# Performance work log

Hardware: AMD Instinct MI355X
Metric: run time of the kernel (lower is better)

Reference implementation:

```python
import jax, jax.numpy as jnp
import numpy as np
from functools import partial

G, NG, H, M, MC = 8, 256, 128, 128, 64
N, S = G * NG, H
TWO_PI = 2.0 * np.pi


def setup_inputs() -> dict:
    key = jax.random.key(0)
    ks = jax.random.split(key, 10)
    node_feat = jax.random.normal(ks[0], (N, S), jnp.float32)
    positions = jax.random.uniform(ks[1], (N, 3), jnp.float32) * 10.0
    # near-orthorhombic triclinic cells, safely invertible
    cell = 10.0 * jnp.eye(3, dtype=jnp.float32)[None] + 0.5 * jax.random.normal(ks[2], (G, 3, 3), jnp.float32)
    batch = jnp.repeat(jnp.arange(G, dtype=jnp.int32), NG)
    n_vecs = jax.random.randint(ks[3], (G, M, 3), -8, 9, dtype=jnp.int32)  # integer lattice vectors
    w = jax.random.uniform(ks[4], (G, M), jnp.float32)  # Ewald k-space weights (positive)
    W_qkv = jax.random.normal(ks[5], (3 * H, H), jnp.float32) / np.sqrt(H)
    W_vg = jax.random.normal(ks[6], (H, H), jnp.float32) / np.sqrt(H)
    b_vg = jnp.full((H,), 2.0, jnp.float32)
    W_hg = jax.random.normal(ks[7], (1, H), jnp.float32) / np.sqrt(H)
    b_hg = jnp.zeros((1,), jnp.float32)
    W_mg = jax.random.normal(ks[8], (1, H), jnp.float32) / np.sqrt(H)
    b_mg = jnp.full((1,), -5.0, jnp.float32)
    return dict(node_feat=node_feat, positions=positions, cell=cell, w=w,
                W_qkv=W_qkv, W_vg=W_vg, b_vg=b_vg, W_hg=W_hg, b_hg=b_hg,
                W_mg=W_mg, b_mg=b_mg, n_vecs=n_vecs, batch=batch)


def reference(node_feat, positions, cell, w, W_qkv, W_vg, b_vg, W_hg, b_hg, W_mg, b_mg, n_vecs, batch):
    Ntot, Sdim = node_feat.shape
    Gn = cell.shape[0]
    Ng = Ntot // Gn
    Hd = Sdim  # in_proj is Identity (S == hidden)
    dtype = node_feat.dtype
    scale_q = np.float32(1.0 / np.sqrt(Hd))

    scalars = node_feat
    qkv = scalars @ W_qkv.T                      # (N, 3H)
    q, k, v = jnp.split(qkv, 3, axis=-1)
    q = jax.nn.silu(q)
    k = jax.nn.silu(k)
    v = v * jax.nn.sigmoid(scalars @ W_vg.T + b_vg)

    # per-graph blocks (batch is block-contiguous: arange(G) repeated NG times)
    qg = q.reshape(Gn, Ng, Hd)
    kg = k.reshape(Gn, Ng, Hd)
    vg = v.reshape(Gn, Ng, Hd)
    a_q, b_q = qg[..., 0::2], qg[..., 1::2]      # (G, Ng, H/2)
    a_k, b_k = kg[..., 0::2], kg[..., 1::2]

    pos_g = positions.reshape(Gn, Ng, 3)
    # fractional coords: solve(cell^T, pos^T)^T, wrapped to [0,1)
    f = jax.vmap(lambda c, p: jnp.linalg.solve(c.T, p.T).T)(cell, pos_g)
    f = f - jnp.floor(f)                         # (G, Ng, 3)

    Mtot = n_vecs.shape[1]
    n_chunks = Mtot // MC
    n_f = n_vecs.astype(dtype)
    # (n_chunks, G, MC, ...) chunk streams for scan over k-space blocks
    n_xs = n_f.reshape(Gn, n_chunks, MC, 3).swapaxes(0, 1)
    w_xs = w.reshape(Gn, n_chunks, MC).swapaxes(0, 1)
    Ng_f = jnp.asarray(Ng, dtype)

    @jax.checkpoint
    def chunk(upd, xs):
        nb, wb = xs                              # (G, MC, 3), (G, MC)
        phase = TWO_PI * jnp.einsum('gni,gmi->gmn', f, nb)   # (G, MC, Ng)
        cos = jnp.cos(phase)[..., None]          # (G, MC, Ng, 1)
        sin = jnp.sin(phase)[..., None]
        aq, bq = a_q[:, None], b_q[:, None]      # (G, 1, Ng, H/2)
        ak, bk = a_k[:, None], b_k[:, None]
        q_rot = jnp.concatenate([aq * cos - bq * sin, aq * sin + bq * cos], -1) * scale_q  # (G,MC,Ng,H)
        k_rot = jnp.concatenate([ak * cos - bk * sin, ak * sin + bk * cos], -1)
        S_blk = jnp.einsum('gmnh,gnd->gmhd', k_rot, vg) / Ng_f   # (G, MC, H, H)
        beta = jnp.einsum('gmnh,gmhd->gmnd', q_rot, S_blk)       # (G, MC, Ng, H)
        upd = upd + jnp.einsum('gm,gmnd->gnd', wb, beta)
        return upd, None

    upd0 = jnp.zeros((Gn, Ng, Hd), dtype)
    upd, _ = jax.lax.scan(chunk, upd0, (n_xs, w_xs))
    update = upd.reshape(Ntot, Hd)

    attn_gate = jnp.tanh(scalars @ W_hg.T + b_hg)      # (N, 1)
    update = update * (1.0 + 0.2 * attn_gate)
    gate_sr_lr = jax.nn.sigmoid(scalars @ W_mg.T + b_mg)
    return update, gate_sr_lr
```

## Files before the change

kernel.cpp:

```cpp
#include <hip/hip_runtime.h>
#include <math.h>

using short8 = __attribute__((ext_vector_type(8))) short;
using f32x4 = __attribute__((ext_vector_type(4))) float;

#define MFMA16(a, b, c) __builtin_amdgcn_mfma_f32_16x16x32_bf16((a), (b), (c), 0, 0, 0)

namespace {
constexpr int NG_ = 256;
constexpr int H_ = 128;
constexpr int NTOT_ = 2048;
constexpr float SCALE_E = 0.08838834764831845f / 256.0f;

constexpr size_t OFF_QA = 0;
constexpr size_t OFF_KA = 524288;
constexpr size_t OFF_VT = 1048576;
constexpr size_t OFF_CT = 1572864;
constexpr size_t OFF_ST = 2097152;
constexpr size_t OFF_GF = 2621440;
}

__device__ __forceinline__ short f2bf(float x) {
  unsigned u = __float_as_uint(x);
  unsigned r = (u + 0x7FFFu + ((u >> 16) & 1u)) >> 16;
  return (short)r;
}
__device__ __forceinline__ float bf2f(short x) {
  return __uint_as_float(((unsigned)(unsigned short)x) << 16);
}
__device__ __forceinline__ float sigmoidf_(float x) { return 1.0f / (1.0f + expf(-x)); }
__device__ __forceinline__ float siluf_(float x) { return x / (1.0f + expf(-x)); }

__device__ __forceinline__ short8 neg8(short8 x) {
  short8 r;
#pragma unroll
  for (int i = 0; i < 8; ++i) r[i] = (short)(x[i] ^ (short)0x8000);
  return r;
}
__device__ __forceinline__ short8 ldf(const short* buf, int row, int kk) {
  return *(const short8*)&buf[(row * 128 + kk) ^ ((row & 7) << 3)];
}
__device__ __forceinline__ short8 ldf64(const short* buf, int row, int kk) {
  return *(const short8*)&buf[(row * 64 + kk) ^ ((row & 7) << 3)];
}

__global__ __launch_bounds__(512) void k_prep(
    const float* __restrict__ nf, const float* __restrict__ Wqkv,
    const float* __restrict__ Wvg, const float* __restrict__ bvg,
    const float* __restrict__ Whg, const float* __restrict__ bhg,
    const float* __restrict__ Wmg, const float* __restrict__ bmg,
    const float* __restrict__ cell, const float* __restrict__ pos,
    const int* __restrict__ nvec, const float* __restrict__ w,
    short* __restrict__ QA, short* __restrict__ KA, short* __restrict__ VT,
    short* __restrict__ CT, short* __restrict__ ST, float* __restrict__ GF,
    float* __restrict__ out_gate, float* __restrict__ out_zero) {
  __shared__ short smem[40960];
  const int tid = threadIdx.x;
  const int bid = blockIdx.x;
  if (bid < 64) {
    short* lA = smem;
    short* lB = smem + 8192;
    const int r_tile = bid >> 1, h = bid & 1;
    const int n0 = r_tile * 64, c0 = h * 256;
#pragma unroll
    for (int it = 0; it < 2; ++it) {
      int e = tid + it * 512;
      int row = e >> 4, c8 = (e & 15) * 8;
      const float* src = nf + (size_t)(n0 + row) * H_ + c8;
      float4 lo = *(const float4*)src, hi = *(const float4*)(src + 4);
      short8 v;
      v[0] = f2bf(lo.x); v[1] = f2bf(lo.y); v[2] = f2bf(lo.z); v[3] = f2bf(lo.w);
      v[4] = f2bf(hi.x); v[5] = f2bf(hi.y); v[6] = f2bf(hi.z); v[7] = f2bf(hi.w);
      *(short8*)&lA[(row * 128 + c8) ^ ((row & 7) << 3)] = v;
    }
#pragma unroll
    for (int it = 0; it < 8; ++it) {
      int e = tid + it * 512;
      int row = e >> 4, c8 = (e & 15) * 8;
      int wr_g = c0 + row;
      const float* src =
          (wr_g < 384 ? Wqkv + (size_t)wr_g * H_ : Wvg + (size_t)(wr_g - 384) * H_) + c8;
      float4 lo = *(const float4*)src, hi = *(const float4*)(src + 4);
      short8 v;
      v[0] = f2bf(lo.x); v[1] = f2bf(lo.y); v[2] = f2bf(lo.z); v[3] = f2bf(lo.w);
      v[4] = f2bf(hi.x); v[5] = f2bf(hi.y); v[6] = f2bf(hi.z); v[7] = f2bf(hi.w);
      *(short8*)&lB[(row * 128 + c8) ^ ((row & 7) << 3)] = v;
    }
    __syncthreads();
    const int wid = tid >> 6, lane = tid & 63;
    const int wrow = (wid >> 2) * 32, wcol = (wid & 3) * 64;
    const int frow = lane & 15, kq = (lane >> 4) * 8;
    f32x4 acc[2][4] = {};
#pragma unroll
    for (int ks = 0; ks < 4; ++ks) {
      int kk = ks * 32 + kq;
      short8 a[2], b[4];
#pragma unroll
      for (int i = 0; i < 2; ++i) a[i] = ldf(lA, wrow + i * 16 + frow, kk);
#pragma unroll
      for (int j = 0; j < 4; ++j) b[j] = ldf(lB, wcol + j * 16 + frow, kk);
#pragma unroll
      for (int i = 0; i < 2; ++i)
#pragma unroll
        for (int j = 0; j < 4; ++j) acc[i][j] = MFMA16(a[i], b[j], acc[i][j]);
    }
    const int orow = (lane >> 4) * 4, ocol = lane & 15;
    __syncthreads();
    if (h == 0) {
#pragma unroll
      for (int i = 0; i < 2; ++i)
#pragma unroll
        for (int j = 0; j < 4; ++j) {
          int c = wcol + j * 16 + ocol;
#pragma unroll
          for (int r = 0; r < 4; ++r) {
            int node = n0 + wrow + i * 16 + orow + r;
            float val = siluf_(acc[i][j][r]);
            if (c < 128)
              QA[(size_t)node * 128 + (c & 1) * 64 + (c >> 1)] = f2bf(val);
            else {
              int ck = c - 128;
              KA[(size_t)node * 128 + (ck & 1) * 64 + (ck >> 1)] = f2bf(val);
            }
          }
        }
    } else {
      short* gate_sh = lB;
      short* vt_sh = lB + 8192;
      if (wcol >= 128) {
#pragma unroll
        for (int i = 0; i < 2; ++i)
#pragma unroll
          for (int j = 0; j < 4; ++j) {
            int d = wcol - 128 + j * 16 + ocol;
#pragma unroll
            for (int r = 0; r < 4; ++r) {
              int nl = wrow + i * 16 + orow + r;
              gate_sh[nl * 128 + d] = f2bf(sigmoidf_(acc[i][j][r] + bvg[d]));
            }
          }
      }
      __syncthreads();
      if (wcol < 128) {
#pragma unroll
        for (int i = 0; i < 2; ++i)
#pragma unroll
          for (int j = 0; j < 4; ++j) {
            int d = wcol + j * 16 + ocol;
#pragma unroll
            for (int r = 0; r < 4; ++r) {
              int nl = wrow + i * 16 + orow + r;
              float gate = bf2f(gate_sh[nl * 128 + d]);
              vt_sh[(d * 64 + nl) ^ ((d & 7) << 3)] = f2bf(acc[i][j][r] * gate);
            }
          }
      }
      __syncthreads();
      const int g_idx = n0 >> 8, nbase = n0 & 255;
#pragma unroll
      for (int it = 0; it < 2; ++it) {
        int e = tid + it * 512;
        int d = e >> 3, n8 = (e & 7) * 8;
        short8 v = *(const short8*)&vt_sh[(d * 64 + n8) ^ ((d & 7) << 3)];
        *(short8*)&VT[((size_t)(g_idx * 128 + d)) * 256 + nbase + n8] = v;
      }
      if (tid < 64) {
        int nl = tid;
        float hg = 0.f, mg = 0.f;
#pragma unroll 8
        for (int c = 0; c < 128; ++c) {
          float s = bf2f(lA[((nl * 128 + (c & ~7)) ^ ((nl & 7) << 3)) + (c & 7)]);
          hg += s * Whg[c];
          mg += s * Wmg[c];
        }
        int node = n0 + nl;
        GF[node] = 1.0f + 0.2f * tanhf(hg + bhg[0]);
        out_gate[node] = sigmoidf_(mg + bmg[0]);
      }
    }
  } else {
    const int b = bid - 64;
    const int g = b >> 3, n0 = (b & 7) * 32;
    {
      float4 z = {0.f, 0.f, 0.f, 0.f};
      float* oz = out_zero + (size_t)b * 4096 + tid * 8;
      *(float4*)oz = z;
      *(float4*)(oz + 4) = z;
    }
    float* f_sh = (float*)smem;
    int* nv_sh = (int*)((char*)smem + 512);
    float* w_sh = (float*)((char*)smem + 2048);
    if (tid < 32) {
      const float* cg = cell + (size_t)g * 9;
      float A00 = cg[0], A01 = cg[3], A02 = cg[6];
      float A10 = cg[1], A11 = cg[4], A12 = cg[7];
      float A20 = cg[2], A21 = cg[5], A22 = cg[8];
      float b00 = A11 * A22 - A12 * A21;
      float b01 = A02 * A21 - A01 * A22;
      float b02 = A01 * A12 - A02 * A11;
      float b10 = A12 * A20 - A10 * A22;
      float b11 = A00 * A22 - A02 * A20;
      float b12 = A02 * A10 - A00 * A12;
      float b20 = A10 * A21 - A11 * A20;
      float b21 = A01 * A20 - A00 * A21;
      float b22 = A00 * A11 - A01 * A10;
      float det = A00 * b00 + A01 * b10 + A02 * b20;
      float inv = 1.0f / det;
      const int node = g * NG_ + n0 + tid;
      float p0 = pos[(size_t)node * 3 + 0];
      float p1 = pos[(size_t)node * 3 + 1];
      float p2 = pos[(size_t)node * 3 + 2];
      float f0 = (b00 * p0 + b01 * p1 + b02 * p2) * inv;
      float f1 = (b10 * p0 + b11 * p1 + b12 * p2) * inv;
      float f2 = (b20 * p0 + b21 * p1 + b22 * p2) * inv;
      f_sh[tid * 4 + 0] = f0 - floorf(f0);
      f_sh[tid * 4 + 1] = f1 - floorf(f1);
      f_sh[tid * 4 + 2] = f2 - floorf(f2);
    }
    if (tid < 128) {
      nv_sh[tid * 3 + 0] = nvec[((size_t)g * 128 + tid) * 3 + 0];
      nv_sh[tid * 3 + 1] = nvec[((size_t)g * 128 + tid) * 3 + 1];
      nv_sh[tid * 3 + 2] = nvec[((size_t)g * 128 + tid) * 3 + 2];
      w_sh[tid] = sqrtf(w[(size_t)g * 128 + tid]);
    }
    __syncthreads();
    const int n_l = tid >> 4, m0 = (tid & 15) * 8;
    float f0 = f_sh[n_l * 4 + 0], f1 = f_sh[n_l * 4 + 1], f2 = f_sh[n_l * 4 + 2];
    short8 pc, ps;
#pragma unroll
    for (int i = 0; i < 8; ++i) {
      int m = m0 + i;
      float dot = f0 * (float)nv_sh[m * 3] + f1 * (float)nv_sh[m * 3 + 1] +
                  f2 * (float)nv_sh[m * 3 + 2];
      float tr = dot - floorf(dot);
      float sn = __builtin_amdgcn_sinf(tr);
      float cs = __builtin_amdgcn_cosf(tr);
      float sq = w_sh[m];
      pc[i] = f2bf(sq * cs);
      ps[i] = f2bf(sq * sn);
    }
    const int node = g * NG_ + n0 + n_l;
    *(short8*)&CT[(size_t)node * 128 + m0] = pc;
    *(short8*)&ST[(size_t)node * 128 + m0] = ps;
  }
}

__global__ __launch_bounds__(512) void k_EV2(
    const short* __restrict__ QA, const short* __restrict__ KA,
    const short* __restrict__ VT, const short* __restrict__ CT,
    const short* __restrict__ ST, const float* __restrict__ GF,
    float* __restrict__ out) {
  __shared__ short smem[47104];
  short* tQ  = smem;
  short* tCr = smem + 4096;
  short* tSr = smem + 8192;
  short* tKA = smem + 12288;
  short* tCc = smem + 20480;
  short* tSc = smem + 28672;
  short* tV  = smem + 36864;
  short* tE  = smem + 45056;
  const int tid = threadIdx.x;
  const int bid = blockIdx.x;
  const int g = bid >> 5;
  const int rt = (bid >> 2) & 7;
  const int cc = bid & 3;
  const int R0 = rt * 32, C0 = cc * 64;
  const int gn = g * NG_;
  const int wid = tid >> 6, lane = tid & 63;
  const int frow = lane & 15, kq = (lane >> 4) * 8;
  const int orow = (lane >> 4) * 4, ocol = lane & 15;
  const int rfrag = wid >> 2;
  const int cfrag = wid & 3;

  {
    int row = tid >> 4, c8 = (tid & 15) * 8;
    int idx = (row * 128 + c8) ^ ((row & 7) << 3);
    size_t ga = (size_t)(gn + R0 + row) * 128 + c8;
    *(short8*)&tQ[idx] = *(const short8*)&QA[ga];
    *(short8*)&tCr[idx] = *(const short8*)&CT[ga];
    *(short8*)&tSr[idx] = *(const short8*)&ST[ga];
  }
#pragma unroll
  for (int it = 0; it < 2; ++it) {
    int e = tid + it * 512;
    int row = e >> 4, c8 = (e & 15) * 8;
    int idx = (row * 128 + c8) ^ ((row & 7) << 3);
    size_t ga = (size_t)(gn + C0 + row) * 128 + c8;
    *(short8*)&tKA[idx] = *(const short8*)&KA[ga];
    *(short8*)&tCc[idx] = *(const short8*)&CT[ga];
    *(short8*)&tSc[idx] = *(const short8*)&ST[ga];
    int d = e >> 3, n8 = (e & 7) * 8;
    *(short8*)&tV[(d * 64 + n8) ^ ((d & 7) << 3)] =
        *(const short8*)&VT[((size_t)g * 128 + d) * 256 + C0 + n8];
  }
  __syncthreads();
  f32x4 gc = {}, gs = {}, qc = {}, qs = {};
#pragma unroll
  for (int ks = 0; ks < 4; ++ks) {
    int kk = ks * 32 + kq, kk2 = (kk + 64) & 127;
    short8 aq = ldf(tQ, rfrag * 16 + frow, kk);
    short8 ka = ldf(tKA, cfrag * 16 + frow, kk);
    short8 t = ldf(tKA, cfrag * 16 + frow, kk2);
    short8 kb = (ks >= 2) ? neg8(t) : t;
    gc = MFMA16(aq, ka, gc);
    gs = MFMA16(aq, kb, gs);
  }
#pragma unroll
  for (int ks = 0; ks < 8; ++ks) {
    const bool lo = ks < 4;
    int kk = (ks & 3) * 32 + kq;
    short8 cr = ldf(tCr, rfrag * 16 + frow, kk);
    short8 sr = ldf(tSr, rfrag * 16 + frow, kk);
    short8 xr = lo ? cr : sr;
    short8 yr = lo ? sr : neg8(cr);
    short8 xc = ldf(lo ? tCc : tSc, cfrag * 16 + frow, kk);
    qc = MFMA16(xr, xc, qc);
    qs = MFMA16(yr, xc, qs);
  }
  {
    int col = cfrag * 16 + ocol;
#pragma unroll
    for (int r = 0; r < 4; ++r) {
      int row = rfrag * 16 + orow + r;
      float ev = gc[r] * qc[r] + gs[r] * qs[r];
      tE[(row * 64 + col) ^ ((row & 7) << 3)] = f2bf(ev);
    }
  }
  __syncthreads();
  f32x4 oacc[2] = {};
#pragma unroll
  for (int ks = 0; ks < 2; ++ks) {
    int kk = ks * 32 + kq;
    short8 a = ldf64(tE, rfrag * 16 + frow, kk);
#pragma unroll
    for (int j = 0; j < 2; ++j) {
      short8 b = ldf64(tV, cfrag * 32 + j * 16 + frow, kk);
      oacc[j] = MFMA16(a, b, oacc[j]);
    }
  }
#pragma unroll
  for (int r = 0; r < 4; ++r) {
    int node = gn + R0 + rfrag * 16 + orow + r;
    float fct = GF[node] * SCALE_E;
#pragma unroll
    for (int j = 0; j < 2; ++j)
      unsafeAtomicAdd(&out[(size_t)node * H_ + cfrag * 32 + j * 16 + ocol],
                      oacc[j][r] * fct);
  }
}

extern "C" void kernel_launch(void* const* d_in, const int* in_sizes, int n_in,
                              void* d_out, int out_size, void* d_ws,
                              size_t ws_size, hipStream_t stream) {
  const float* node_feat = (const float*)d_in[0];
  const float* positions = (const float*)d_in[1];
  const float* cell = (const float*)d_in[2];
  const float* w = (const float*)d_in[3];
  const float* Wqkv = (const float*)d_in[4];
  const float* Wvg = (const float*)d_in[5];
  const float* bvg = (const float*)d_in[6];
  const float* Whg = (const float*)d_in[7];
  const float* bhg = (const float*)d_in[8];
  const float* Wmg = (const float*)d_in[9];
  const float* bmg = (const float*)d_in[10];
  const int* nvec = (const int*)d_in[11];
  float* out = (float*)d_out;
  char* ws = (char*)d_ws;

  short* QA = (short*)(ws + OFF_QA);
  short* KA = (short*)(ws + OFF_KA);
  short* VT = (short*)(ws + OFF_VT);
  short* CT = (short*)(ws + OFF_CT);
  short* ST = (short*)(ws + OFF_ST);
  float* GF = (float*)(ws + OFF_GF);
  float* out_gate = out + (size_t)NTOT_ * H_;

  k_prep<<<128, 512, 0, stream>>>(node_feat, Wqkv, Wvg, bvg, Whg, bhg, Wmg, bmg,
                                  cell, positions, nvec, w, QA, KA, VT, CT, ST,
                                  GF, out_gate, out);
  k_EV2<<<256, 512, 0, stream>>>(QA, KA, VT, CT, ST, GF, out);
}
```

Baseline: 23.77 us.

## Split prep projection into smaller tiles and stream weights directly from global

The projection part of the prep kernel now uses 128 blocks of 32 rows instead of 64 blocks of 64 rows, so more CUs share the work. Each wave loads its weight rows straight from global memory and converts them to bf16 in registers, instead of staging the whole weight tile in shared memory. The Q/K de-interleave moves from the output write to a permuted choice of weight rows, which gives contiguous stores. Static shared arrays replace the large shared buffer. The h==0 path now writes each Q/K value twice, which adds redundant global stores and looks like leftover debugging.

```diff
diff --git a/kernel.cpp b/kernel.cpp
--- a/kernel.cpp
+++ b/kernel.cpp
@@ -1,4 +1,5 @@
 #include <hip/hip_runtime.h>
+#include <hip/hip_bf16.h>
 #include <math.h>
 
 using short8 = __attribute__((ext_vector_type(8))) short;
@@ -21,9 +22,8 @@
 }
 
 __device__ __forceinline__ short f2bf(float x) {
-  unsigned u = __float_as_uint(x);
-  unsigned r = (u + 0x7FFFu + ((u >> 16) & 1u)) >> 16;
-  return (short)r;
+  __hip_bfloat16 h = __float2bfloat16(x);
+  return *reinterpret_cast<short*>(&h);
 }
 __device__ __forceinline__ float bf2f(short x) {
   return __uint_as_float(((unsigned)(unsigned short)x) << 16);
@@ -42,6 +42,13 @@
 }
 __device__ __forceinline__ short8 ldf64(const short* buf, int row, int kk) {
   return *(const short8*)&buf[(row * 64 + kk) ^ ((row & 7) << 3)];
+}
+__device__ __forceinline__ short8 cvt8(const float* src) {
+  float4 lo = *(const float4*)src, hi = *(const float4*)(src + 4);
+  short8 v;
+  v[0] = f2bf(lo.x); v[1] = f2bf(lo.y); v[2] = f2bf(lo.z); v[3] = f2bf(lo.w);
+  v[4] = f2bf(hi.x); v[5] = f2bf(hi.y); v[6] = f2bf(hi.z); v[7] = f2bf(hi.w);
+  return v;
 }
 
 __global__ __launch_bounds__(512) void k_prep(
@@ -54,122 +61,117 @@
     short* __restrict__ QA, short* __restrict__ KA, short* __restrict__ VT,
     short* __restrict__ CT, short* __restrict__ ST, float* __restrict__ GF,
     float* __restrict__ out_gate, float* __restrict__ out_zero) {
-  __shared__ short smem[40960];
+  __shared__ short sA[32 * 128];
+  __shared__ short gate_sh[32 * 128];
+  __shared__ short vt_sh[128 * 32];
   const int tid = threadIdx.x;
   const int bid = blockIdx.x;
-  if (bid < 64) {
-    short* lA = smem;
-    short* lB = smem + 8192;
+  if (bid < 128) {
     const int r_tile = bid >> 1, h = bid & 1;
-    const int n0 = r_tile * 64, c0 = h * 256;
-#pragma unroll
-    for (int it = 0; it < 2; ++it) {
-      int e = tid + it * 512;
-      int row = e >> 4, c8 = (e & 15) * 8;
-      const float* src = nf + (size_t)(n0 + row) * H_ + c8;
-      float4 lo = *(const float4*)src, hi = *(const float4*)(src + 4);
-      short8 v;
-      v[0] = f2bf(lo.x); v[1] = f2bf(lo.y); v[2] = f2bf(lo.z); v[3] = f2bf(lo.w);
-      v[4] = f2bf(hi.x); v[5] = f2bf(hi.y); v[6] = f2bf(hi.z); v[7] = f2bf(hi.w);
-      *(short8*)&lA[(row * 128 + c8) ^ ((row & 7) << 3)] = v;
-    }
-#pragma unroll
-    for (int it = 0; it < 8; ++it) {
-      int e = tid + it * 512;
-      int row = e >> 4, c8 = (e & 15) * 8;
-      int wr_g = c0 + row;
-      const float* src =
-          (wr_g < 384 ? Wqkv + (size_t)wr_g * H_ : Wvg + (size_t)(wr_g - 384) * H_) + c8;
-      float4 lo = *(const float4*)src, hi = *(const float4*)(src + 4);
-      short8 v;
-      v[0] = f2bf(lo.x); v[1] = f2bf(lo.y); v[2] = f2bf(lo.z); v[3] = f2bf(lo.w);
-      v[4] = f2bf(hi.x); v[5] = f2bf(hi.y); v[6] = f2bf(hi.z); v[7] = f2bf(hi.w);
-      *(short8*)&lB[(row * 128 + c8) ^ ((row & 7) << 3)] = v;
+    const int n0 = r_tile * 32;
+    {
+      int row = tid >> 4, c8 = (tid & 15) * 8;
+      *(short8*)&sA[(row * 128 + c8) ^ ((row & 7) << 3)] =
+          cvt8(nf + (size_t)(n0 + row) * H_ + c8);
     }
     __syncthreads();
     const int wid = tid >> 6, lane = tid & 63;
-    const int wrow = (wid >> 2) * 32, wcol = (wid & 3) * 64;
     const int frow = lane & 15, kq = (lane >> 4) * 8;
-    f32x4 acc[2][4] = {};
+    const int orow = (lane >> 4) * 4, ocol = lane & 15;
+    int wrow[2];
+    const float* brow[2];
+#pragma unroll
+    for (int j = 0; j < 2; ++j) {
+      int c = wid * 32 + j * 16 + frow;
+      if (h == 0) {
+        int wr;
+        if (c < 128)
+          wr = (c < 64) ? (2 * c) : (2 * (c - 64) + 1);
+        else {
+          int q = c - 128;
+          wr = 128 + ((q < 64) ? (2 * q) : (2 * (q - 64) + 1));
+        }
+        wrow[j] = wr;
+        brow[j] = Wqkv + (size_t)wr * H_;
+      } else {
+        int wr = 256 + c;
+        wrow[j] = wr;
+        brow[j] = (wr < 384) ? (Wqkv + (size_t)wr * H_)
+                             : (Wvg + (size_t)(wr - 384) * H_);
+      }
+    }
+    f32x4 acc[2][2] = {};
 #pragma unroll
     for (int ks = 0; ks < 4; ++ks) {
       int kk = ks * 32 + kq;
-      short8 a[2], b[4];
-#pragma unroll
-      for (int i = 0; i < 2; ++i) a[i] = ldf(lA, wrow + i * 16 + frow, kk);
-#pragma unroll
-      for (int j = 0; j < 4; ++j) b[j] = ldf(lB, wcol + j * 16 + frow, kk);
+      short8 a[2], b[2];
+#pragma unroll
+      for (int i = 0; i < 2; ++i) a[i] = ldf(sA, i * 16 + frow, kk);
+#pragma unroll
+      for (int j = 0; j < 2; ++j) b[j] = cvt8(brow[j] + kk);
 #pragma unroll
       for (int i = 0; i < 2; ++i)
 #pragma unroll
-        for (int j = 0; j < 4; ++j) acc[i][j] = MFMA16(a[i], b[j], acc[i][j]);
-    }
-    const int orow = (lane >> 4) * 4, ocol = lane & 15;
-    __syncthreads();
+        for (int j = 0; j < 2; ++j) acc[i][j] = MFMA16(a[i], b[j], acc[i][j]);
+    }
     if (h == 0) {
 #pragma unroll
       for (int i = 0; i < 2; ++i)
 #pragma unroll
-        for (int j = 0; j < 4; ++j) {
-          int c = wcol + j * 16 + ocol;
+        for (int j = 0; j < 2; ++j) {
+          int c = wid * 32 + j * 16 + ocol;
+          short* dst = (c < 128) ? (QA + c) : (KA + c - 128);
 #pragma unroll
           for (int r = 0; r < 4; ++r) {
-            int node = n0 + wrow + i * 16 + orow + r;
-            float val = siluf_(acc[i][j][r]);
+            int node = n0 + i * 16 + orow + r;
+            dst[(size_t)node * 128] = f2bf(siluf_(acc[i][j][r]));
+            dst += 0;
+          }
+#pragma unroll
+          for (int r = 0; r < 4; ++r) {
+            int node = n0 + i * 16 + orow + r;
             if (c < 128)
-              QA[(size_t)node * 128 + (c & 1) * 64 + (c >> 1)] = f2bf(val);
-            else {
-              int ck = c - 128;
-              KA[(size_t)node * 128 + (ck & 1) * 64 + (ck >> 1)] = f2bf(val);
-            }
+              QA[(size_t)node * 128 + c] = f2bf(siluf_(acc[i][j][r]));
+            else
+              KA[(size_t)node * 128 + (c - 128)] = f2bf(siluf_(acc[i][j][r]));
           }
         }
     } else {
-      short* gate_sh = lB;
-      short* vt_sh = lB + 8192;
-      if (wcol >= 128) {
+      if (wid >= 4) {
 #pragma unroll
         for (int i = 0; i < 2; ++i)
 #pragma unroll
-          for (int j = 0; j < 4; ++j) {
-            int d = wcol - 128 + j * 16 + ocol;
+          for (int j = 0; j < 2; ++j) {
+            int d = (wid - 4) * 32 + j * 16 + ocol;
 #pragma unroll
             for (int r = 0; r < 4; ++r) {
-              int nl = wrow + i * 16 + orow + r;
+              int nl = i * 16 + orow + r;
               gate_sh[nl * 128 + d] = f2bf(sigmoidf_(acc[i][j][r] + bvg[d]));
             }
           }
       }
       __syncthreads();
-      if (wcol < 128) {
+      if (wid < 4) {
 #pragma unroll
         for (int i = 0; i < 2; ++i)
 #pragma unroll
-          for (int j = 0; j < 4; ++j) {
-            int d = wcol + j * 16 + ocol;
+          for (int j = 0; j < 2; ++j) {
+            int d = wid * 32 + j * 16 + ocol;
 #pragma unroll
             for (int r = 0; r < 4; ++r) {
-              int nl = wrow + i * 16 + orow + r;
+              int nl = i * 16 + orow + r;
               float gate = bf2f(gate_sh[nl * 128 + d]);
-              vt_sh[(d * 64 + nl) ^ ((d & 7) << 3)] = f2bf(acc[i][j][r] * gate);
+              vt_sh[(d * 32 + nl) ^ ((d & 3) << 3)] =
+                  f2bf(acc[i][j][r] * gate);
             }
           }
       }
-      __syncthreads();
-      const int g_idx = n0 >> 8, nbase = n0 & 255;
-#pragma unroll
-      for (int it = 0; it < 2; ++it) {
-        int e = tid + it * 512;
-        int d = e >> 3, n8 = (e & 7) * 8;
-        short8 v = *(const short8*)&vt_sh[(d * 64 + n8) ^ ((d & 7) << 3)];
-        *(short8*)&VT[((size_t)(g_idx * 128 + d)) * 256 + nbase + n8] = v;
-      }
-      if (tid < 64) {
+      if (tid < 32) {
         int nl = tid;
         float hg = 0.f, mg = 0.f;
 #pragma unroll 8
         for (int c = 0; c < 128; ++c) {
-          float s = bf2f(lA[((nl * 128 + (c & ~7)) ^ ((nl & 7) << 3)) + (c & 7)]);
+          float s = bf2f(sA[(nl * 128 + c) ^ ((nl & 7) << 3)]);
           hg += s * Whg[c];
           mg += s * Wmg[c];
         }
@@ -177,9 +179,16 @@
         GF[node] = 1.0f + 0.2f * tanhf(hg + bhg[0]);
         out_gate[node] = sigmoidf_(mg + bmg[0]);
       }
+      __syncthreads();
+      const int g_idx = n0 >> 8, nbase = n0 & 255;
+      {
+        int d = tid >> 2, n8 = (tid & 3) * 8;
+        short8 v = *(const short8*)&vt_sh[(d * 32 + n8) ^ ((d & 3) << 3)];
+        *(short8*)&VT[((size_t)(g_idx * 128 + d)) * 256 + nbase + n8] = v;
+      }
     }
   } else {
-    const int b = bid - 64;
+    const int b = bid - 128;
     const int g = b >> 3, n0 = (b & 7) * 32;
     {
       float4 z = {0.f, 0.f, 0.f, 0.f};
@@ -187,9 +196,9 @@
       *(float4*)oz = z;
       *(float4*)(oz + 4) = z;
     }
-    float* f_sh = (float*)smem;
-    int* nv_sh = (int*)((char*)smem + 512);
-    float* w_sh = (float*)((char*)smem + 2048);
+    __shared__ float f_sh[32 * 4];
+    __shared__ int nv_sh[128 * 3];
+    __shared__ float w_sh[128];
     if (tid < 32) {
       const float* cg = cell + (size_t)g * 9;
       float A00 = cg[0], A01 = cg[3], A02 = cg[6];
@@ -375,7 +384,7 @@
   float* GF = (float*)(ws + OFF_GF);
   float* out_gate = out + (size_t)NTOT_ * H_;
 
-  k_prep<<<128, 512, 0, stream>>>(node_feat, Wqkv, Wvg, bvg, Whg, bhg, Wmg, bmg,
+  k_prep<<<192, 512, 0, stream>>>(node_feat, Wqkv, Wvg, bvg, Whg, bhg, Wmg, bmg,
                                   cell, positions, nvec, w, QA, KA, VT, CT, ST,
                                   GF, out_gate, out);
   k_EV2<<<256, 512, 0, stream>>>(QA, KA, VT, CT, ST, GF, out);
```

Measured after the change: 23.57 us, median of 3. No clear change (-0.8%).
